# Performance work log

Measured on AMD Instinct MI355X. Metric: run time of the kernel, lower is better.

## Reference

```python
import jax, jax.numpy as jnp
import numpy as np

NUM_CLASSES = 512


def setup_inputs() -> dict:
    key = jax.random.key(0)
    k1, k2 = jax.random.split(key)
    support_data = jax.random.normal(k1, (2560, 64, 5, 5), dtype=jnp.float32)
    query_data = jax.random.normal(k2, (8192, 64, 5, 5), dtype=jnp.float32)
    # every class 0..511 appears exactly 5 times (sorted, like unique() ordering)
    support_label = (jnp.arange(2560, dtype=jnp.int32) // 5).astype(jnp.int32)
    return {"support_data": support_data, "query_data": query_data,
            "support_label": support_label}


def reference(support_data, query_data, support_label):
    # embedding_net == identity: embeddings are the raw (N, C, H, W) tensors.
    n_q = query_data.shape[0]
    d = support_data.shape[1] * support_data.shape[2] * support_data.shape[3]
    s = support_data.reshape(support_data.shape[0], d)   # [Ns, d]
    q = query_data.reshape(n_q, d)                        # [Nq, d]

    # class-mean prototypes (scatter-mean == per-unique-label mean loop)
    sums = jax.ops.segment_sum(s, support_label, num_segments=NUM_CLASSES)      # [M, d]
    counts = jax.ops.segment_sum(jnp.ones((s.shape[0],), s.dtype),
                                 support_label, num_segments=NUM_CLASSES)       # [M]
    protos = sums / counts[:, None]                                             # [M, d]

    # squared euclidean distance: ||q||^2 + ||p||^2 - 2 q.p  (same math as
    # broadcast (q - p)**2 summed over c,h,w, without the [Nq,M,d] intermediate)
    q2 = jnp.sum(q * q, axis=1, keepdims=True)            # [Nq, 1]
    p2 = jnp.sum(protos * protos, axis=1)                 # [M]
    dist = q2 + p2[None, :] - 2.0 * (q @ protos.T)        # [Nq, M]

    return jax.nn.log_softmax(-dist, axis=1)
```

## Files before the change

kernel.cpp:

```cpp
#include <hip/hip_runtime.h>
#include <hip/hip_bf16.h>
#include <cstdint>
#include <cstddef>

#define NS 2560
#define NQ 8192
#define NC 512
#define DD 1600

typedef __bf16 bf16_t;
typedef __bf16 bf16x4 __attribute__((ext_vector_type(4)));
typedef __bf16 bf16x8 __attribute__((ext_vector_type(8)));
typedef float f32x4 __attribute__((ext_vector_type(4)));

__global__ __launch_bounds__(256) void proto_kernel(
    const float* __restrict__ sup, const int* __restrict__ lab,
    bf16_t* __restrict__ protos, float* __restrict__ p2)
{
    const int m   = blockIdx.x;
    const int tid = threadIdx.x;
    __shared__ int   idxs[32];
    __shared__ int   cnt;
    __shared__ float wsum[4];
    if (tid == 0) cnt = 0;
    __syncthreads();
    for (int i = tid; i < NS; i += 256) {
        if (lab[i] == m) {
            int p = atomicAdd(&cnt, 1);
            if (p < 32) idxs[p] = i;
        }
    }
    __syncthreads();
    int n = cnt < 32 ? cnt : 32;
    if (tid == 0 && n > 1) {
        for (int a = 1; a < n; ++a) {
            int key = idxs[a]; int b = a - 1;
            while (b >= 0 && idxs[b] > key) { idxs[b+1] = idxs[b]; --b; }
            idxs[b+1] = key;
        }
    }
    __syncthreads();

    float acc[7];
    #pragma unroll
    for (int u = 0; u < 7; ++u) acc[u] = 0.f;
    for (int t = 0; t < n; ++t) {
        const float* src = sup + (size_t)idxs[t] * DD;
        #pragma unroll
        for (int u = 0; u < 7; ++u) {
            int j = tid + u * 256;
            if (j < DD) acc[u] += src[j];
        }
    }
    float inv = (n > 0) ? 1.f / (float)n : 0.f;
    float psq = 0.f;
    #pragma unroll
    for (int u = 0; u < 7; ++u) {
        int j = tid + u * 256;
        if (j < DD) {
            float p = acc[u] * inv;
            bf16_t pb = (bf16_t)p;
            protos[(size_t)m * DD + j] = pb;
            float pf = (float)pb;
            psq += pf * pf;
        }
    }
    #pragma unroll
    for (int o = 32; o > 0; o >>= 1) psq += __shfl_xor(psq, o);
    int lane = tid & 63, wid = tid >> 6;
    if (lane == 0) wsum[wid] = psq;
    __syncthreads();
    if (tid == 0) p2[m] = wsum[0] + wsum[1] + wsum[2] + wsum[3];
}

__device__ __forceinline__ void stage_B(const bf16_t* __restrict__ protos,
                                        bf16_t* bbuf, int k0, int tid, int wid)
{
    #pragma unroll
    for (int p = 0; p < 8; ++p) {
        int idx = p * 512 + tid;
        int row = idx >> 3;
        int gs  = (idx & 7) ^ (row & 7);
        const bf16_t* src = protos + (size_t)row * DD + k0 + gs * 8;
        char* dst = (char*)bbuf + (size_t)(p * 512 + wid * 64) * 16;
        __builtin_amdgcn_global_load_lds(
            (const __attribute__((address_space(1))) void*)src,
            (__attribute__((address_space(3))) void*)dst, 16, 0, 0);
    }
}

__global__ __launch_bounds__(512, 2) void fused_kernel(
    const float* __restrict__ q, const bf16_t* __restrict__ protos,
    const float* __restrict__ p2, float* __restrict__ out)
{
    extern __shared__ char smem[];
    bf16_t* Bs0 = (bf16_t*)(smem);
    bf16_t* Bs1 = (bf16_t*)(smem + 65536);
    bf16_t* As0 = (bf16_t*)(smem + 131072);
    bf16_t* As1 = (bf16_t*)(smem + 135168);

    const int tid  = threadIdx.x;
    const int lane = tid & 63;
    const int wid  = tid >> 6;
    const int r    = lane & 15;
    const int g    = lane >> 4;
    const int m0   = blockIdx.x * 32;

    float p2c[4];
    #pragma unroll
    for (int ni = 0; ni < 4; ++ni) p2c[ni] = p2[wid * 64 + ni * 16 + r];

    f32x4 acc[2][4];
    #pragma unroll
    for (int mi = 0; mi < 2; ++mi)
        #pragma unroll
        for (int ni = 0; ni < 4; ++ni)
            acc[mi][ni] = (f32x4){0.f, 0.f, 0.f, 0.f};

    const int arow = tid >> 4;
    const int acg  = tid & 15;
    const float* aptr = q + (size_t)(m0 + arow) * DD + acg * 4;
    const int    aoff = (arow * 128 + acg * 8) ^ ((arow & 7) << 4);

    {
        float4 f = *(const float4*)(aptr);
        stage_B(protos, Bs0, 0, tid, wid);
        bf16x4 w;
        w[0] = (bf16_t)f.x; w[1] = (bf16_t)f.y; w[2] = (bf16_t)f.z; w[3] = (bf16_t)f.w;
        *(bf16x4*)((char*)As0 + aoff) = w;
        __syncthreads();
    }

    for (int t = 0; t < 25; ++t) {
        const int cur = t & 1;
        bf16_t* bs  = cur ? Bs1 : Bs0;
        bf16_t* as  = cur ? As1 : As0;
        bf16_t* bsn = cur ? Bs0 : Bs1;
        bf16_t* asn = cur ? As0 : As1;
        const bool pre = (t < 24);

        float4 fA;
        if (pre) {
            fA = *(const float4*)(aptr + (t + 1) * 64);
            stage_B(protos, bsn, (t + 1) * 64, tid, wid);
        }

        #pragma unroll
        for (int kk = 0; kk < 2; ++kk) {
            bf16x8 af[2], bfr[4];
            #pragma unroll
            for (int mi = 0; mi < 2; ++mi) {
                int ab = ((mi * 16 + r) * 128 + kk * 64 + g * 16) ^ ((r & 7) << 4);
                af[mi] = *(const bf16x8*)((const char*)as + ab);
            }
            #pragma unroll
            for (int ni = 0; ni < 4; ++ni) {
                int c  = wid * 64 + ni * 16 + r;
                int bb = (c * 128 + kk * 64 + g * 16) ^ ((r & 7) << 4);
                bfr[ni] = *(const bf16x8*)((const char*)bs + bb);
            }
            #pragma unroll
            for (int mi = 0; mi < 2; ++mi)
                #pragma unroll
                for (int ni = 0; ni < 4; ++ni)
                    acc[mi][ni] = __builtin_amdgcn_mfma_f32_16x16x32_bf16(
                        af[mi], bfr[ni], acc[mi][ni], 0, 0, 0);
        }

        if (pre) {
            bf16x4 w;
            w[0] = (bf16_t)fA.x; w[1] = (bf16_t)fA.y;
            w[2] = (bf16_t)fA.z; w[3] = (bf16_t)fA.w;
            *(bf16x4*)((char*)asn + aoff) = w;
        }
        __syncthreads();
    }

    #pragma unroll
    for (int mi = 0; mi < 2; ++mi)
        #pragma unroll
        for (int ni = 0; ni < 4; ++ni)
            #pragma unroll
            for (int j = 0; j < 4; ++j)
                acc[mi][ni][j] = 2.f * acc[mi][ni][j] - p2c[ni];

    float* red  = (float*)smem;
    float* gmax = red + 256;
    float* lse  = gmax + 32;

    float rmax[2][4];
    #pragma unroll
    for (int mi = 0; mi < 2; ++mi)
        #pragma unroll
        for (int j = 0; j < 4; ++j) {
            float m = acc[mi][0][j];
            #pragma unroll
            for (int ni = 1; ni < 4; ++ni) m = fmaxf(m, acc[mi][ni][j]);
            rmax[mi][j] = m;
        }
    #pragma unroll
    for (int o = 1; o < 16; o <<= 1)
        #pragma unroll
        for (int mi = 0; mi < 2; ++mi)
            #pragma unroll
            for (int j = 0; j < 4; ++j)
                rmax[mi][j] = fmaxf(rmax[mi][j], __shfl_xor(rmax[mi][j], o));
    if (r == 0) {
        #pragma unroll
        for (int mi = 0; mi < 2; ++mi)
            #pragma unroll
            for (int j = 0; j < 4; ++j)
                red[(mi * 16 + g * 4 + j) * 8 + wid] = rmax[mi][j];
    }
    __syncthreads();
    if (tid < 32) {
        float m = red[tid * 8];
        #pragma unroll
        for (int w = 1; w < 8; ++w) m = fmaxf(m, red[tid * 8 + w]);
        gmax[tid] = m;
    }
    __syncthreads();

    float rsum[2][4];
    #pragma unroll
    for (int mi = 0; mi < 2; ++mi)
        #pragma unroll
        for (int j = 0; j < 4; ++j) {
            float gm = gmax[mi * 16 + g * 4 + j];
            float s = 0.f;
            #pragma unroll
            for (int ni = 0; ni < 4; ++ni) s += expf(acc[mi][ni][j] - gm);
            rsum[mi][j] = s;
        }
    #pragma unroll
    for (int o = 1; o < 16; o <<= 1)
        #pragma unroll
        for (int mi = 0; mi < 2; ++mi)
            #pragma unroll
            for (int j = 0; j < 4; ++j)
                rsum[mi][j] += __shfl_xor(rsum[mi][j], o);
    if (r == 0) {
        #pragma unroll
        for (int mi = 0; mi < 2; ++mi)
            #pragma unroll
            for (int j = 0; j < 4; ++j)
                red[(mi * 16 + g * 4 + j) * 8 + wid] = rsum[mi][j];
    }
    __syncthreads();
    if (tid < 32) {
        float s = 0.f;
        #pragma unroll
        for (int w = 0; w < 8; ++w) s += red[tid * 8 + w];
        lse[tid] = gmax[tid] + logf(s);
    }
    __syncthreads();

    #pragma unroll
    for (int mi = 0; mi < 2; ++mi) {
        #pragma unroll
        for (int j = 0; j < 4; ++j) {
            float l = lse[mi * 16 + g * 4 + j];
            size_t rowoff = (size_t)(m0 + mi * 16 + g * 4 + j) * NC;
            #pragma unroll
            for (int ni = 0; ni < 4; ++ni)
                out[rowoff + wid * 64 + ni * 16 + r] = acc[mi][ni][j] - l;
        }
    }
}

extern "C" void kernel_launch(void* const* d_in, const int* in_sizes, int n_in,
                              void* d_out, int out_size, void* d_ws, size_t ws_size,
                              hipStream_t stream)
{
    const float* sup = (const float*)d_in[0];
    const float* qry = (const float*)d_in[1];
    const int*   lab = (const int*)d_in[2];
    float* out = (float*)d_out;

    char* ws = (char*)d_ws;
    bf16_t* protos = (bf16_t*)ws;
    float*  p2     = (float*)(ws + 1638400);

    const int smem_bytes = 139264;
    hipFuncSetAttribute(reinterpret_cast<const void*>(fused_kernel),
                        hipFuncAttributeMaxDynamicSharedMemorySize, smem_bytes);

    proto_kernel<<<NC, 256, 0, stream>>>(sup, lab, protos, p2);
    fused_kernel<<<NQ / 32, 512, smem_bytes, stream>>>(qry, protos, p2, out);
}
```

Baseline: 54.76 us.

## Make B staging wave-private and replace syncthreads with partial vmcnt waits

Each wave now fetches only the 64 prototype rows it consumes into its own LDS strip, so B tiles no longer need to be visible across waves. This lets the loop swap __syncthreads for an lgkmcnt-only wait plus s_barrier, and a vmcnt(9) wait that keeps the next tile's global-to-LDS loads in flight during the MFMA work instead of draining them every iteration. sched_barriers pin the instruction ordering. The gain is more load/compute overlap; the risk is that correctness now depends on hand-written waitcnt counts matching the issue order.

```diff
diff --git a/kernel.cpp b/kernel.cpp
--- a/kernel.cpp
+++ b/kernel.cpp
@@ -73,16 +73,17 @@
     if (tid == 0) p2[m] = wsum[0] + wsum[1] + wsum[2] + wsum[3];
 }
 
-__device__ __forceinline__ void stage_B(const bf16_t* __restrict__ protos,
-                                        bf16_t* bbuf, int k0, int tid, int wid)
+__device__ __forceinline__ void stage_B_wave(const bf16_t* __restrict__ protos,
+                                             char* strip, int k0, int lane, int wid)
 {
     #pragma unroll
     for (int p = 0; p < 8; ++p) {
-        int idx = p * 512 + tid;
-        int row = idx >> 3;
-        int gs  = (idx & 7) ^ (row & 7);
-        const bf16_t* src = protos + (size_t)row * DD + k0 + gs * 8;
-        char* dst = (char*)bbuf + (size_t)(p * 512 + wid * 64) * 16;
+        int gidx = p * 64 + lane;
+        int row  = gidx >> 3;
+        int gcol = gidx & 7;
+        const bf16_t* src = protos + (size_t)(wid * 64 + row) * DD + k0
+                          + ((gcol ^ (row & 7)) * 8);
+        char* dst = strip + p * 1024;
         __builtin_amdgcn_global_load_lds(
             (const __attribute__((address_space(1))) void*)src,
             (__attribute__((address_space(3))) void*)dst, 16, 0, 0);
@@ -94,10 +95,6 @@
     const float* __restrict__ p2, float* __restrict__ out)
 {
     extern __shared__ char smem[];
-    bf16_t* Bs0 = (bf16_t*)(smem);
-    bf16_t* Bs1 = (bf16_t*)(smem + 65536);
-    bf16_t* As0 = (bf16_t*)(smem + 131072);
-    bf16_t* As1 = (bf16_t*)(smem + 135168);
 
     const int tid  = threadIdx.x;
     const int lane = tid & 63;
@@ -124,26 +121,35 @@
 
     {
         float4 f = *(const float4*)(aptr);
-        stage_B(protos, Bs0, 0, tid, wid);
+        __builtin_amdgcn_sched_barrier(0);
+        stage_B_wave(protos, smem + wid * 8192, 0, lane, wid);
+        __builtin_amdgcn_sched_barrier(0);
         bf16x4 w;
         w[0] = (bf16_t)f.x; w[1] = (bf16_t)f.y; w[2] = (bf16_t)f.z; w[3] = (bf16_t)f.w;
-        *(bf16x4*)((char*)As0 + aoff) = w;
-        __syncthreads();
+        *(bf16x4*)(smem + 131072 + aoff) = w;
+        asm volatile("s_waitcnt lgkmcnt(0)" ::: "memory");
+        __builtin_amdgcn_sched_barrier(0);
+        __builtin_amdgcn_s_barrier();
+        __builtin_amdgcn_sched_barrier(0);
     }
 
     for (int t = 0; t < 25; ++t) {
         const int cur = t & 1;
-        bf16_t* bs  = cur ? Bs1 : Bs0;
-        bf16_t* as  = cur ? As1 : As0;
-        bf16_t* bsn = cur ? Bs0 : Bs1;
-        bf16_t* asn = cur ? As0 : As1;
-        const bool pre = (t < 24);
+        const char* bstrip  = smem + cur * 65536 + wid * 8192;
+        char*       bstripn = smem + (cur ^ 1) * 65536 + wid * 8192;
+        const char* as      = smem + 131072 + cur * 4096;
+        char*       asn     = smem + 131072 + (cur ^ 1) * 4096;
+        const bool  pre     = (t < 24);
 
         float4 fA;
-        if (pre) {
-            fA = *(const float4*)(aptr + (t + 1) * 64);
-            stage_B(protos, bsn, (t + 1) * 64, tid, wid);
-        }
+        if (pre) fA = *(const float4*)(aptr + (t + 1) * 64);
+        __builtin_amdgcn_sched_barrier(0);
+        if (pre) stage_B_wave(protos, bstripn, (t + 1) * 64, lane, wid);
+        __builtin_amdgcn_sched_barrier(0);
+
+        if (pre) asm volatile("s_waitcnt vmcnt(9)" ::: "memory");
+        else     asm volatile("s_waitcnt vmcnt(0)" ::: "memory");
+        __builtin_amdgcn_sched_barrier(0);
 
         #pragma unroll
         for (int kk = 0; kk < 2; ++kk) {
@@ -151,13 +157,13 @@
             #pragma unroll
             for (int mi = 0; mi < 2; ++mi) {
                 int ab = ((mi * 16 + r) * 128 + kk * 64 + g * 16) ^ ((r & 7) << 4);
-                af[mi] = *(const bf16x8*)((const char*)as + ab);
+                af[mi] = *(const bf16x8*)(as + ab);
             }
             #pragma unroll
             for (int ni = 0; ni < 4; ++ni) {
-                int c  = wid * 64 + ni * 16 + r;
-                int bb = (c * 128 + kk * 64 + g * 16) ^ ((r & 7) << 4);
-                bfr[ni] = *(const bf16x8*)((const char*)bs + bb);
+                int c  = ni * 16 + r;
+                int bb = (c * 128 + kk * 64 + g * 16) ^ ((c & 7) << 4);
+                bfr[ni] = *(const bf16x8*)(bstrip + bb);
             }
             #pragma unroll
             for (int mi = 0; mi < 2; ++mi)
@@ -171,9 +177,12 @@
             bf16x4 w;
             w[0] = (bf16_t)fA.x; w[1] = (bf16_t)fA.y;
             w[2] = (bf16_t)fA.z; w[3] = (bf16_t)fA.w;
-            *(bf16x4*)((char*)asn + aoff) = w;
-        }
-        __syncthreads();
+            *(bf16x4*)(asn + aoff) = w;
+        }
+        asm volatile("s_waitcnt lgkmcnt(0)" ::: "memory");
+        __builtin_amdgcn_sched_barrier(0);
+        __builtin_amdgcn_s_barrier();
+        __builtin_amdgcn_sched_barrier(0);
     }
 
     #pragma unroll
```

Measured after the change: 60.71 us. +10.9%, slower.
